# Kernel optimization log

Measured on AMD Instinct MI355X. Metric: run time of the kernel, lower is better.

The kernel has to match this reference:

```python
import jax, jax.numpy as jnp
import numpy as np

WINDOW_SIZE = 512
CAUSAL = True

def _sliding_window_mask(seq_len, window_size, causal):
    i = jnp.arange(seq_len)[:, None]
    j = jnp.arange(seq_len)[None, :]
    mask = (j >= i - window_size + 1) & (j <= i)
    if causal:
        mask = mask & (j <= i)
    return mask  # [S, S] bool, True = attend


def setup_inputs() -> dict:
    key = jax.random.key(0)
    k1, k2, k3 = jax.random.split(key, 3)
    B, S, D = 16, 4096, 64
    q = jax.random.normal(k1, (B, S, D), dtype=jnp.float32)
    k = jax.random.normal(k2, (B, S, D), dtype=jnp.float32)
    v = jax.random.normal(k3, (B, S, D), dtype=jnp.float32)
    return {"q": q, "k": k, "v": v}


def reference(q, k, v):
    B, S, D = q.shape
    scale = D ** -0.5
    mask = _sliding_window_mask(S, WINDOW_SIZE, CAUSAL)  # [S, S]
    scores = jnp.einsum("bqd,bkd->bqk", q, k) * scale    # [B, S, S]
    mask_value = -jnp.finfo(scores.dtype).max
    scores = jnp.where(mask[None, :, :], scores, mask_value)
    attn = jax.nn.softmax(scores, axis=-1)
    out = jnp.einsum("bqk,bkd->bqd", attn, v)            # [B, S, D]
    return out
```

## Files before the change

### kernel.cpp

```cpp
#include <hip/hip_runtime.h>
#include <hip/hip_bf16.h>

#define BATCH 16
#define SEQ   4096
#define DIM   64
#define WIN   512

constexpr int BM = 64;
constexpr int BN = 64;
constexpr int PAD = 8;
constexpr float QSCALE = 0.125f * 1.44269504088896340736f;

typedef __bf16 bf16x8 __attribute__((ext_vector_type(8)));
typedef float  f32x4  __attribute__((ext_vector_type(4)));

__global__ __launch_bounds__(256)
void swa_fa_kernel(const float* __restrict__ qg, const float* __restrict__ kg,
                   const float* __restrict__ vg, float* __restrict__ outg) {
    __shared__ __bf16 Qsh[BM][DIM + PAD];
    __shared__ __bf16 Ksh[BN][DIM + PAD];
    __shared__ __bf16 Vsh[DIM][BN + PAD];
    __shared__ __bf16 Psh[4][16][BN + PAD];

    const int tid  = threadIdx.x;
    const int lane = tid & 63;
    const int wave = tid >> 6;
    const int lr   = lane & 15;
    const int quad = lane >> 4;

    const int b     = blockIdx.y;
    const int qblk  = blockIdx.x;
    const int qrow0 = qblk * BM;

    const float* qb = qg + (size_t)b * SEQ * DIM;
    const float* kb = kg + (size_t)b * SEQ * DIM;
    const float* vb = vg + (size_t)b * SEQ * DIM;

    #pragma unroll
    for (int i = 0; i < 4; ++i) {
        const int fid = tid + 256 * i;
        const int row = fid >> 4;
        const int c4  = (fid & 15) * 4;
        const float4 qv = *(const float4*)&qb[(size_t)(qrow0 + row) * DIM + c4];
        Qsh[row][c4 + 0] = (__bf16)(qv.x * QSCALE);
        Qsh[row][c4 + 1] = (__bf16)(qv.y * QSCALE);
        Qsh[row][c4 + 2] = (__bf16)(qv.z * QSCALE);
        Qsh[row][c4 + 3] = (__bf16)(qv.w * QSCALE);
    }
    __syncthreads();

    const bf16x8 qa0 = *(const bf16x8*)&Qsh[wave * 16 + lr][quad * 8];
    const bf16x8 qa1 = *(const bf16x8*)&Qsh[wave * 16 + lr][32 + quad * 8];

    const int wr0      = qrow0 + wave * 16;
    const int row_base = wr0 + quad * 4;

    f32x4 o[4];
    #pragma unroll
    for (int n = 0; n < 4; ++n) o[n] = (f32x4){0.f, 0.f, 0.f, 0.f};
    float m_run[4], l_run[4];
    #pragma unroll
    for (int r = 0; r < 4; ++r) { m_run[r] = -1e30f; l_run[r] = 0.f; }

    const int t0 = (qrow0 - (WIN - 1)) > 0 ? (qrow0 - (WIN - 1)) >> 6 : 0;
    const int t1 = qblk;

    for (int t = t0; t <= t1; ++t) {
        __syncthreads();
        #pragma unroll
        for (int i = 0; i < 4; ++i) {
            const int fid = tid + 256 * i;
            const int row = fid >> 4;
            const int c4  = (fid & 15) * 4;
            const size_t goff = (size_t)(t * BN + row) * DIM + c4;
            const float4 kv = *(const float4*)&kb[goff];
            Ksh[row][c4 + 0] = (__bf16)kv.x;
            Ksh[row][c4 + 1] = (__bf16)kv.y;
            Ksh[row][c4 + 2] = (__bf16)kv.z;
            Ksh[row][c4 + 3] = (__bf16)kv.w;
            const float4 vv = *(const float4*)&vb[goff];
            Vsh[c4 + 0][row] = (__bf16)vv.x;
            Vsh[c4 + 1][row] = (__bf16)vv.y;
            Vsh[c4 + 2][row] = (__bf16)vv.z;
            Vsh[c4 + 3][row] = (__bf16)vv.w;
        }
        __syncthreads();

        if (t * BN + (BN - 1) + (WIN - 1) < wr0) continue;

        f32x4 sc[4];
        #pragma unroll
        for (int n = 0; n < 4; ++n) {
            const bf16x8 kf0 = *(const bf16x8*)&Ksh[n * 16 + lr][quad * 8];
            const bf16x8 kf1 = *(const bf16x8*)&Ksh[n * 16 + lr][32 + quad * 8];
            f32x4 s = (f32x4){0.f, 0.f, 0.f, 0.f};
            s = __builtin_amdgcn_mfma_f32_16x16x32_bf16(qa0, kf0, s, 0, 0, 0);
            s = __builtin_amdgcn_mfma_f32_16x16x32_bf16(qa1, kf1, s, 0, 0, 0);
            sc[n] = s;
        }

        float mt[4];
        #pragma unroll
        for (int r = 0; r < 4; ++r) mt[r] = -1e30f;
        #pragma unroll
        for (int n = 0; n < 4; ++n) {
            const int key = t * BN + n * 16 + lr;
            #pragma unroll
            for (int r = 0; r < 4; ++r) {
                const int row = row_base + r;
                const float sv = ((unsigned)(row - key) < (unsigned)WIN) ? sc[n][r] : -1e30f;
                sc[n][r] = sv;
                mt[r] = fmaxf(mt[r], sv);
            }
        }
        #pragma unroll
        for (int off = 1; off < 16; off <<= 1) {
            #pragma unroll
            for (int r = 0; r < 4; ++r)
                mt[r] = fmaxf(mt[r], __shfl_xor(mt[r], off));
        }
        float al[4];
        #pragma unroll
        for (int r = 0; r < 4; ++r) {
            const float mn = fmaxf(m_run[r], mt[r]);
            al[r] = exp2f(m_run[r] - mn);
            m_run[r] = mn;
            l_run[r] *= al[r];
        }
        #pragma unroll
        for (int n = 0; n < 4; ++n) {
            #pragma unroll
            for (int r = 0; r < 4; ++r) {
                const float p = exp2f(sc[n][r] - m_run[r]);
                l_run[r] += p;
                Psh[wave][quad * 4 + r][n * 16 + lr] = (__bf16)p;
            }
        }
        #pragma unroll
        for (int n = 0; n < 4; ++n) {
            #pragma unroll
            for (int r = 0; r < 4; ++r) o[n][r] *= al[r];
        }
        const bf16x8 pa0 = *(const bf16x8*)&Psh[wave][lr][quad * 8];
        const bf16x8 pa1 = *(const bf16x8*)&Psh[wave][lr][32 + quad * 8];
        #pragma unroll
        for (int n = 0; n < 4; ++n) {
            const bf16x8 vf0 = *(const bf16x8*)&Vsh[n * 16 + lr][quad * 8];
            const bf16x8 vf1 = *(const bf16x8*)&Vsh[n * 16 + lr][32 + quad * 8];
            o[n] = __builtin_amdgcn_mfma_f32_16x16x32_bf16(pa0, vf0, o[n], 0, 0, 0);
            o[n] = __builtin_amdgcn_mfma_f32_16x16x32_bf16(pa1, vf1, o[n], 0, 0, 0);
        }
    }

    #pragma unroll
    for (int off = 1; off < 16; off <<= 1) {
        #pragma unroll
        for (int r = 0; r < 4; ++r)
            l_run[r] += __shfl_xor(l_run[r], off);
    }
    float* ob = outg + (size_t)b * SEQ * DIM;
    #pragma unroll
    for (int r = 0; r < 4; ++r) {
        const float inv = 1.0f / l_run[r];
        const int row = row_base + r;
        #pragma unroll
        for (int n = 0; n < 4; ++n) {
            ob[(size_t)row * DIM + n * 16 + lr] = o[n][r] * inv;
        }
    }
}

extern "C" void kernel_launch(void* const* d_in, const int* in_sizes, int n_in,
                              void* d_out, int out_size, void* d_ws, size_t ws_size,
                              hipStream_t stream) {
    (void)in_sizes; (void)n_in; (void)out_size; (void)d_ws; (void)ws_size;
    const float* q = (const float*)d_in[0];
    const float* k = (const float*)d_in[1];
    const float* v = (const float*)d_in[2];
    float* out = (float*)d_out;
    dim3 grid(SEQ / BM, BATCH);
    swa_fa_kernel<<<grid, dim3(256), 0, stream>>>(q, k, v, out);
}
```

Before: 131.1 us.

## Transpose score MFMA to keep P in registers, switch to fp16, stage output

```diff
diff --git a/kernel.cpp b/kernel.cpp
--- a/kernel.cpp
+++ b/kernel.cpp
@@ -1,5 +1,4 @@
 #include <hip/hip_runtime.h>
-#include <hip/hip_bf16.h>
 
 #define BATCH 16
 #define SEQ   4096
@@ -8,19 +7,28 @@
 
 constexpr int BM = 64;
 constexpr int BN = 64;
-constexpr int PAD = 8;
-constexpr float QSCALE = 0.125f * 1.44269504088896340736f;
+constexpr int KS = DIM + 8;
+constexpr int VS = BN + 4;
+constexpr int OS = DIM + 4;
+constexpr float QSCALE  = 0.125f * 1.44269504088896340736f;
+constexpr float MASKVAL = -3.0e38f;
 
-typedef __bf16 bf16x8 __attribute__((ext_vector_type(8)));
-typedef float  f32x4  __attribute__((ext_vector_type(4)));
+typedef _Float16 f16x2 __attribute__((ext_vector_type(2)));
+typedef _Float16 f16x4 __attribute__((ext_vector_type(4)));
+typedef _Float16 f16x8 __attribute__((ext_vector_type(8)));
+typedef float    f32x4 __attribute__((ext_vector_type(4)));
+
+__device__ __forceinline__ f16x2 pk2(float a, float b) {
+    return __builtin_bit_cast(f16x2, __builtin_amdgcn_cvt_pkrtz(a, b));
+}
 
 __global__ __launch_bounds__(256)
-void swa_fa_kernel(const float* __restrict__ qg, const float* __restrict__ kg,
-                   const float* __restrict__ vg, float* __restrict__ outg) {
-    __shared__ __bf16 Qsh[BM][DIM + PAD];
-    __shared__ __bf16 Ksh[BN][DIM + PAD];
-    __shared__ __bf16 Vsh[DIM][BN + PAD];
-    __shared__ __bf16 Psh[4][16][BN + PAD];
+void swa_kernel(const float* __restrict__ qg, const float* __restrict__ kg,
+                const float* __restrict__ vg, float* __restrict__ outg) {
+    __shared__ __align__(16) char smem[(BN * KS + DIM * VS) * 2];
+    _Float16* Ksh = (_Float16*)smem;
+    _Float16* Vsh = (_Float16*)(smem + BN * KS * 2);
+    float*    Osh = (float*)smem;
 
     const int tid  = threadIdx.x;
     const int lane = tid & 63;
@@ -31,38 +39,36 @@
     const int b     = blockIdx.y;
     const int qblk  = blockIdx.x;
     const int qrow0 = qblk * BM;
+    const int wr0   = qrow0 + wave * 16;
+    const int q     = wr0 + lr;
 
     const float* qb = qg + (size_t)b * SEQ * DIM;
     const float* kb = kg + (size_t)b * SEQ * DIM;
     const float* vb = vg + (size_t)b * SEQ * DIM;
+    float*       ob = outg + (size_t)b * SEQ * DIM;
 
-    #pragma unroll
-    for (int i = 0; i < 4; ++i) {
-        const int fid = tid + 256 * i;
-        const int row = fid >> 4;
-        const int c4  = (fid & 15) * 4;
-        const float4 qv = *(const float4*)&qb[(size_t)(qrow0 + row) * DIM + c4];
-        Qsh[row][c4 + 0] = (__bf16)(qv.x * QSCALE);
-        Qsh[row][c4 + 1] = (__bf16)(qv.y * QSCALE);
-        Qsh[row][c4 + 2] = (__bf16)(qv.z * QSCALE);
-        Qsh[row][c4 + 3] = (__bf16)(qv.w * QSCALE);
-    }
-    __syncthreads();
-
-    const bf16x8 qa0 = *(const bf16x8*)&Qsh[wave * 16 + lr][quad * 8];
-    const bf16x8 qa1 = *(const bf16x8*)&Qsh[wave * 16 + lr][32 + quad * 8];
-
-    const int wr0      = qrow0 + wave * 16;
-    const int row_base = wr0 + quad * 4;
+    const float* qp = qb + (size_t)q * DIM + quad * 8;
+    const float4 a0 = *(const float4*)(qp + 0);
+    const float4 a1 = *(const float4*)(qp + 4);
+    const float4 a2 = *(const float4*)(qp + 32);
+    const float4 a3 = *(const float4*)(qp + 36);
+    union { f16x8 v; f16x2 h[4]; } uq0, uq1;
+    uq0.h[0] = pk2(a0.x * QSCALE, a0.y * QSCALE);
+    uq0.h[1] = pk2(a0.z * QSCALE, a0.w * QSCALE);
+    uq0.h[2] = pk2(a1.x * QSCALE, a1.y * QSCALE);
+    uq0.h[3] = pk2(a1.z * QSCALE, a1.w * QSCALE);
+    uq1.h[0] = pk2(a2.x * QSCALE, a2.y * QSCALE);
+    uq1.h[1] = pk2(a2.z * QSCALE, a2.w * QSCALE);
+    uq1.h[2] = pk2(a3.x * QSCALE, a3.y * QSCALE);
+    uq1.h[3] = pk2(a3.z * QSCALE, a3.w * QSCALE);
+    const f16x8 qf0 = uq0.v, qf1 = uq1.v;
 
     f32x4 o[4];
     #pragma unroll
-    for (int n = 0; n < 4; ++n) o[n] = (f32x4){0.f, 0.f, 0.f, 0.f};
-    float m_run[4], l_run[4];
-    #pragma unroll
-    for (int r = 0; r < 4; ++r) { m_run[r] = -1e30f; l_run[r] = 0.f; }
+    for (int mi = 0; mi < 4; ++mi) o[mi] = (f32x4){0.f, 0.f, 0.f, 0.f};
+    float m_run = -1e30f, l_run = 0.f;
 
-    const int t0 = (qrow0 - (WIN - 1)) > 0 ? (qrow0 - (WIN - 1)) >> 6 : 0;
+    const int t0 = (qrow0 > (WIN - 1)) ? (qrow0 - (WIN - 1)) >> 6 : 0;
     const int t1 = qblk;
 
     for (int t = t0; t <= t1; ++t) {
@@ -72,101 +78,104 @@
             const int fid = tid + 256 * i;
             const int row = fid >> 4;
             const int c4  = (fid & 15) * 4;
-            const size_t goff = (size_t)(t * BN + row) * DIM + c4;
-            const float4 kv = *(const float4*)&kb[goff];
-            Ksh[row][c4 + 0] = (__bf16)kv.x;
-            Ksh[row][c4 + 1] = (__bf16)kv.y;
-            Ksh[row][c4 + 2] = (__bf16)kv.z;
-            Ksh[row][c4 + 3] = (__bf16)kv.w;
-            const float4 vv = *(const float4*)&vb[goff];
-            Vsh[c4 + 0][row] = (__bf16)vv.x;
-            Vsh[c4 + 1][row] = (__bf16)vv.y;
-            Vsh[c4 + 2][row] = (__bf16)vv.z;
-            Vsh[c4 + 3][row] = (__bf16)vv.w;
+            const size_t g = (size_t)(t * BN + row) * DIM + c4;
+            const float4 kv = *(const float4*)&kb[g];
+            union { f16x4 v; f16x2 h[2]; } uk;
+            uk.h[0] = pk2(kv.x, kv.y);
+            uk.h[1] = pk2(kv.z, kv.w);
+            *(f16x4*)&Ksh[row * KS + c4] = uk.v;
+            const float4 vv = *(const float4*)&vb[g];
+            Vsh[(c4 + 0) * VS + row] = (_Float16)vv.x;
+            Vsh[(c4 + 1) * VS + row] = (_Float16)vv.y;
+            Vsh[(c4 + 2) * VS + row] = (_Float16)vv.z;
+            Vsh[(c4 + 3) * VS + row] = (_Float16)vv.w;
         }
         __syncthreads();
 
-        if (t * BN + (BN - 1) + (WIN - 1) < wr0) continue;
+        if (t * BN + (BN - 1) < wr0 - (WIN - 1)) continue;
+        const int kbase = t * BN;
 
         f32x4 sc[4];
         #pragma unroll
-        for (int n = 0; n < 4; ++n) {
-            const bf16x8 kf0 = *(const bf16x8*)&Ksh[n * 16 + lr][quad * 8];
-            const bf16x8 kf1 = *(const bf16x8*)&Ksh[n * 16 + lr][32 + quad * 8];
+        for (int mt = 0; mt < 4; ++mt) {
+            const f16x8 kf0 = *(const f16x8*)&Ksh[(mt * 16 + lr) * KS + quad * 8];
+            const f16x8 kf1 = *(const f16x8*)&Ksh[(mt * 16 + lr) * KS + 32 + quad * 8];
             f32x4 s = (f32x4){0.f, 0.f, 0.f, 0.f};
-            s = __builtin_amdgcn_mfma_f32_16x16x32_bf16(qa0, kf0, s, 0, 0, 0);
-            s = __builtin_amdgcn_mfma_f32_16x16x32_bf16(qa1, kf1, s, 0, 0, 0);
-            sc[n] = s;
+            s = __builtin_amdgcn_mfma_f32_16x16x32_f16(kf0, qf0, s, 0, 0, 0);
+            s = __builtin_amdgcn_mfma_f32_16x16x32_f16(kf1, qf1, s, 0, 0, 0);
+            sc[mt] = s;
         }
 
-        float mt[4];
-        #pragma unroll
-        for (int r = 0; r < 4; ++r) mt[r] = -1e30f;
-        #pragma unroll
-        for (int n = 0; n < 4; ++n) {
-            const int key = t * BN + n * 16 + lr;
+        const bool edge = (kbase < wr0 + 15 - (WIN - 1)) || (kbase + BN - 1 > wr0);
+        if (edge) {
             #pragma unroll
-            for (int r = 0; r < 4; ++r) {
-                const int row = row_base + r;
-                const float sv = ((unsigned)(row - key) < (unsigned)WIN) ? sc[n][r] : -1e30f;
-                sc[n][r] = sv;
-                mt[r] = fmaxf(mt[r], sv);
+            for (int mt = 0; mt < 4; ++mt) {
+                #pragma unroll
+                for (int r = 0; r < 4; ++r) {
+                    const int key = kbase + mt * 16 + quad * 4 + r;
+                    sc[mt][r] = ((unsigned)(q - key) < (unsigned)WIN) ? sc[mt][r] : MASKVAL;
+                }
             }
         }
+
+        float mt_ = MASKVAL;
         #pragma unroll
-        for (int off = 1; off < 16; off <<= 1) {
+        for (int mtile = 0; mtile < 4; ++mtile)
             #pragma unroll
-            for (int r = 0; r < 4; ++r)
-                mt[r] = fmaxf(mt[r], __shfl_xor(mt[r], off));
+            for (int r = 0; r < 4; ++r) mt_ = fmaxf(mt_, sc[mtile][r]);
+        mt_ = fmaxf(mt_, __shfl_xor(mt_, 16));
+        mt_ = fmaxf(mt_, __shfl_xor(mt_, 32));
+        const float mn    = fmaxf(m_run, mt_);
+        const float alpha = exp2f(m_run - mn);
+        m_run = mn;
+
+        f16x4 pb[4];
+        float ls = 0.f;
+        #pragma unroll
+        for (int nt = 0; nt < 4; ++nt) {
+            const float p0 = exp2f(sc[nt][0] - mn);
+            const float p1 = exp2f(sc[nt][1] - mn);
+            const float p2 = exp2f(sc[nt][2] - mn);
+            const float p3 = exp2f(sc[nt][3] - mn);
+            ls += (p0 + p1) + (p2 + p3);
+            union { f16x4 v; f16x2 h[2]; } up;
+            up.h[0] = pk2(p0, p1);
+            up.h[1] = pk2(p2, p3);
+            pb[nt] = up.v;
         }
-        float al[4];
+        l_run = l_run * alpha + ls;
         #pragma unroll
-        for (int r = 0; r < 4; ++r) {
-            const float mn = fmaxf(m_run[r], mt[r]);
-            al[r] = exp2f(m_run[r] - mn);
-            m_run[r] = mn;
-            l_run[r] *= al[r];
-        }
+        for (int mi = 0; mi < 4; ++mi) o[mi] = o[mi] * alpha;
+
         #pragma unroll
-        for (int n = 0; n < 4; ++n) {
+        for (int nt = 0; nt < 4; ++nt) {
             #pragma unroll
-            for (int r = 0; r < 4; ++r) {
-                const float p = exp2f(sc[n][r] - m_run[r]);
-                l_run[r] += p;
-                Psh[wave][quad * 4 + r][n * 16 + lr] = (__bf16)p;
+            for (int mi = 0; mi < 4; ++mi) {
+                const f16x4 vf = *(const f16x4*)&Vsh[(mi * 16 + lr) * VS + nt * 16 + quad * 4];
+                o[mi] = __builtin_amdgcn_mfma_f32_16x16x16f16(vf, pb[nt], o[mi], 0, 0, 0);
             }
-        }
-        #pragma unroll
-        for (int n = 0; n < 4; ++n) {
-            #pragma unroll
-            for (int r = 0; r < 4; ++r) o[n][r] *= al[r];
-        }
-        const bf16x8 pa0 = *(const bf16x8*)&Psh[wave][lr][quad * 8];
-        const bf16x8 pa1 = *(const bf16x8*)&Psh[wave][lr][32 + quad * 8];
-        #pragma unroll
-        for (int n = 0; n < 4; ++n) {
-            const bf16x8 vf0 = *(const bf16x8*)&Vsh[n * 16 + lr][quad * 8];
-            const bf16x8 vf1 = *(const bf16x8*)&Vsh[n * 16 + lr][32 + quad * 8];
-            o[n] = __builtin_amdgcn_mfma_f32_16x16x32_bf16(pa0, vf0, o[n], 0, 0, 0);
-            o[n] = __builtin_amdgcn_mfma_f32_16x16x32_bf16(pa1, vf1, o[n], 0, 0, 0);
         }
     }
 
+    l_run += __shfl_xor(l_run, 16);
+    l_run += __shfl_xor(l_run, 32);
+    const float inv = 1.0f / l_run;
+
+    __syncthreads();
+    float* Ow = Osh + wave * 16 * OS;
     #pragma unroll
-    for (int off = 1; off < 16; off <<= 1) {
-        #pragma unroll
-        for (int r = 0; r < 4; ++r)
-            l_run[r] += __shfl_xor(l_run[r], off);
+    for (int mi = 0; mi < 4; ++mi) {
+        float4 st;
+        st.x = o[mi][0] * inv; st.y = o[mi][1] * inv;
+        st.z = o[mi][2] * inv; st.w = o[mi][3] * inv;
+        *(float4*)&Ow[lr * OS + mi * 16 + quad * 4] = st;
     }
-    float* ob = outg + (size_t)b * SEQ * DIM;
     #pragma unroll
-    for (int r = 0; r < 4; ++r) {
-        const float inv = 1.0f / l_run[r];
-        const int row = row_base + r;
-        #pragma unroll
-        for (int n = 0; n < 4; ++n) {
-            ob[(size_t)row * DIM + n * 16 + lr] = o[n][r] * inv;
-        }
+    for (int j = 0; j < 4; ++j) {
+        const int qq = quad + 4 * j;
+        const int d4 = lr * 4;
+        const float4 vst = *(const float4*)&Ow[qq * OS + d4];
+        *(float4*)&ob[(size_t)(wr0 + qq) * DIM + d4] = vst;
     }
 }
 
@@ -179,5 +188,5 @@
     const float* v = (const float*)d_in[2];
     float* out = (float*)d_out;
     dim3 grid(SEQ / BM, BATCH);
-    swa_fa_kernel<<<grid, dim3(256), 0, stream>>>(q, k, v, out);
+    swa_kernel<<<grid, dim3(256), 0, stream>>>(q, k, v, out);
 }
```

Measured after the change: 129.2 us. Within noise of the previous version (-1.4%).
